# Performance work log

Hardware: AMD Instinct MI355X
Metric: run time of the kernel (lower is better)

Reference implementation:

```python
import jax, jax.numpy as jnp
import numpy as np

N = 8192
D_IN = 128
D_HID = 256  # hard-coded nn.Linear(input_dim, 256) in the module
D_OUT = 64
BN_EPS = 1e-5
LEAKY_SLOPE = 0.01


def setup_inputs() -> dict:
    key = jax.random.key(0)
    k_h, k_a, k_wt, k_wo = jax.random.split(key, 4)
    H = jax.random.normal(k_h, (N, D_IN), dtype=jnp.float32)
    # Fixed adjacency passed to __init__; values in [0,1) so mask=ceil(A*1e-5) is {0,1}
    A = jax.random.uniform(k_a, (N, N), dtype=jnp.float32)
    bn_weight = jnp.ones((D_IN,), jnp.float32)
    bn_bias = jnp.zeros((D_IN,), jnp.float32)
    W_theta = jax.random.normal(k_wt, (D_IN, D_HID), jnp.float32) * np.float32(1.0 / np.sqrt(D_IN))
    b_theta = jnp.zeros((D_HID,), jnp.float32)
    W_out = jax.random.normal(k_wo, (D_IN, D_OUT), jnp.float32) * np.float32(1.0 / np.sqrt(D_IN))
    b_out = jnp.zeros((D_OUT,), jnp.float32)
    return {"H": H, "A": A, "bn_weight": bn_weight, "bn_bias": bn_bias,
            "W_theta": W_theta, "b_theta": b_theta, "W_out": W_out, "b_out": b_out}


def reference(H, A, bn_weight, bn_bias, W_theta, b_theta, W_out, b_out):
    # BatchNorm1d in training mode: biased batch statistics over the node dim
    mean = jnp.mean(H, axis=0)
    var = jnp.mean(jnp.square(H - mean), axis=0)
    Hn = (H - mean) * jax.lax.rsqrt(var + BN_EPS) * bn_weight + bn_bias  # [N, D_IN]

    Hx = Hn @ W_theta + b_theta  # [N, 256]
    mask = jnp.ceil(A * 1e-5)    # constant {0,1} mask from fixed adjacency

    # Dynamic adjacency: clamp(sigmoid(Hx Hx^T), min=0.1) * mask + I
    S = jnp.clip(jax.nn.sigmoid(Hx @ Hx.T), 0.1, None)  # [N, N]
    Ad = S * mask + jnp.eye(N, dtype=H.dtype)

    # D^{-1/2} A D^{-1/2} via broadcast scaling (same math as diag matmuls)
    d = jax.lax.rsqrt(jnp.sum(Ad, axis=1))  # D^{-0.5}, [N]
    A_hat = Ad * d[:, None] * d[None, :]

    out = A_hat @ (Hn @ W_out + b_out)       # [N, D_OUT]
    out = jnp.where(out >= 0, out, LEAKY_SLOPE * out)  # LeakyReLU(0.01)
    return out, A_hat
```

## Files before the change

kernel.cpp:

```cpp
#include <hip/hip_runtime.h>
#include <hip/hip_bf16.h>

#define N 8192
#define DIN 128
#define DHID 256
#define DOUT 64
#define VP 136

typedef __attribute__((ext_vector_type(8))) short short8;
typedef __attribute__((ext_vector_type(8))) unsigned short u16x8;
typedef __attribute__((ext_vector_type(4))) float f32x4;
typedef __attribute__((ext_vector_type(2))) unsigned long long u64x2;

typedef __attribute__((address_space(1))) const unsigned int GlbU32;
typedef __attribute__((address_space(3))) unsigned int LdsU32;

__device__ inline void gload16(const void* g, void* l) {
  __builtin_amdgcn_global_load_lds((GlbU32*)g, (LdsU32*)l, 16, 0, 0);
}

#define LGKM_BAR()                                            \
  do {                                                        \
    asm volatile("s_waitcnt lgkmcnt(0)" ::: "memory");        \
    __builtin_amdgcn_sched_barrier(0);                        \
    __builtin_amdgcn_s_barrier();                             \
    __builtin_amdgcn_sched_barrier(0);                        \
  } while (0)

__device__ inline unsigned short f2bf(float x) {
  unsigned u = __float_as_uint(x);
  u += 0x7FFF + ((u >> 16) & 1);
  return (unsigned short)(u >> 16);
}
__device__ inline float bf2f(unsigned short u) {
  return __uint_as_float(((unsigned)u) << 16);
}
__device__ inline float sig_clip(float x) {
  float s = 1.0f / (1.0f + __expf(-x));
  return fmaxf(s, 0.1f);
}

__global__ __launch_bounds__(256) void maskpack(const float* __restrict__ A,
                                                unsigned long long* __restrict__ Mb) {
  size_t i = (size_t)blockIdx.x * 256 + threadIdx.x;
  size_t step = (size_t)gridDim.x * 256;
  int l = threadIdx.x & 63;
  for (; i < (size_t)N * N / 4; i += step) {
    f32x4 a = *(const f32x4*)&A[i * 4];
    unsigned long long b0 = __ballot(a[0] > 0.f);
    unsigned long long b1 = __ballot(a[1] > 0.f);
    unsigned long long b2 = __ballot(a[2] > 0.f);
    unsigned long long b3 = __ballot(a[3] > 0.f);
    size_t g = (i - l) >> 6;
    if (l < 4) {
      unsigned long long bb = (l == 0) ? b0 : (l == 1) ? b1 : (l == 2) ? b2 : b3;
      Mb[g * 4 + l] = bb;
    }
  }
}

__global__ void bn_stats(const float* __restrict__ H, const float* __restrict__ bnw,
                         const float* __restrict__ bnb, float* __restrict__ scale,
                         float* __restrict__ shift) {
  int f = blockIdx.x;
  int t = threadIdx.x;
  float s = 0.f, sq = 0.f;
  for (int r = t; r < N; r += 256) {
    float v = H[(size_t)r * DIN + f];
    s += v; sq += v * v;
  }
  __shared__ float ss[256], s2[256];
  ss[t] = s; s2[t] = sq;
  __syncthreads();
  for (int o = 128; o > 0; o >>= 1) {
    if (t < o) { ss[t] += ss[t + o]; s2[t] += s2[t + o]; }
    __syncthreads();
  }
  if (t == 0) {
    float mean = ss[0] * (1.0f / N);
    float var = s2[0] * (1.0f / N) - mean * mean;
    float sc = rsqrtf(var + 1e-5f) * bnw[f];
    scale[f] = sc;
    shift[f] = bnb[f] - mean * sc;
  }
}

__global__ __launch_bounds__(256) void proj(const float* __restrict__ H,
                     const float* __restrict__ scale, const float* __restrict__ shift,
                     const float* __restrict__ Wt, const float* __restrict__ bt,
                     const float* __restrict__ Wo, const float* __restrict__ bo,
                     unsigned short* __restrict__ Hx, unsigned short* __restrict__ M2T) {
  __shared__ float hn[8][DIN];
  int i0 = blockIdx.x * 8;
  int t = threadIdx.x;
  #pragma unroll
  for (int rep = 0; rep < 4; ++rep) {
    int idx = rep * 256 + t;
    int r = idx >> 7, c = idx & 127;
    float h = H[(size_t)(i0 + r) * DIN + c];
    hn[r][c] = fmaf(h, scale[c], shift[c]);
  }
  __syncthreads();
  {
    int c = t;
    float acc[8];
    float b = bt[c];
    #pragma unroll
    for (int r = 0; r < 8; ++r) acc[r] = b;
    for (int k = 0; k < DIN; ++k) {
      float w = Wt[k * DHID + c];
      #pragma unroll
      for (int r = 0; r < 8; ++r) acc[r] = fmaf(hn[r][k], w, acc[r]);
    }
    #pragma unroll
    for (int r = 0; r < 8; ++r) Hx[(size_t)(i0 + r) * DHID + c] = f2bf(acc[r]);
  }
  if (t < DOUT) {
    int c = t;
    float acc[8];
    float b = bo[c];
    #pragma unroll
    for (int r = 0; r < 8; ++r) acc[r] = b;
    for (int k = 0; k < DIN; ++k) {
      float w = Wo[k * DOUT + c];
      #pragma unroll
      for (int r = 0; r < 8; ++r) acc[r] = fmaf(hn[r][k], w, acc[r]);
    }
    u16x8 v;
    #pragma unroll
    for (int r = 0; r < 8; ++r) v[r] = f2bf(acc[r]);
    *(u16x8*)&M2T[(size_t)c * N + i0] = v;
  }
}

__global__ __launch_bounds__(256, 3) void rsum(const unsigned short* __restrict__ Hx,
                     const unsigned long long* __restrict__ Mb,
                     float* __restrict__ rowsum) {
  __shared__ unsigned short lsh[24576];
  __shared__ unsigned mbt32[64][4];
  unsigned short* lA = lsh;
  unsigned short* lb = lsh + 16384;
  const int blk = blockIdx.x;
  const int jq = blk & 7;
  const int it = blk >> 3;
  const int i0 = it * 64;
  const int t = threadIdx.x;
  const int w = t >> 6, l = t & 63;
  const int lr = l & 15, lg = l >> 4;
  const int srow = l >> 3;
  const int scol = ((l & 7) ^ srow) * 8;
  const int fswz = (lr & 7) * 8;

  #pragma unroll
  for (int itr = 0; itr < 8; ++itr) {
    int idx = itr * 4 + w;
    int c4 = idx >> 3, rg = idx & 7;
    int row = rg * 8 + srow;
    gload16(&Hx[(size_t)(i0 + row) * DHID + c4 * 64 + scol], &lA[idx * 512]);
  }
  if (t < 128) {
    int j0 = jq * 1024;
    int mrow = t >> 1, ep = (t & 1) * 2;
    u64x2 mv = *(const u64x2*)&Mb[(size_t)(i0 + mrow) * (N / 64) + (j0 >> 8) * 4 + ep];
    int sh = (j0 & 128) ? 32 : 0;
    mbt32[mrow][ep] = (unsigned)(mv[0] >> sh);
    mbt32[mrow][ep + 1] = (unsigned)(mv[1] >> sh);
  }
  __syncthreads();

  float rs[4] = {0.f, 0.f, 0.f, 0.f};
  f32x4 zero = {0.f, 0.f, 0.f, 0.f};

  for (int jtl = 0; jtl < 8; ++jtl) {
    const int j0 = (jq * 8 + jtl) * 128;
    f32x4 acc[8];
    #pragma unroll
    for (int n = 0; n < 8; ++n) acc[n] = zero;

    #pragma unroll
    for (int c4 = 0; c4 < 4; ++c4) {
      __syncthreads();
      #pragma unroll
      for (int itr = 0; itr < 4; ++itr) {
        int rg = itr * 4 + w;
        int row = rg * 8 + srow;
        gload16(&Hx[(size_t)(j0 + row) * DHID + c4 * 64 + scol], &lb[rg * 512]);
      }
      __syncthreads();
      #pragma unroll
      for (int kk = 0; kk < 2; ++kk) {
        int c = (kk * 32 + lg * 8) ^ fswz;
        short8 a0 = *(const short8*)&lA[c4 * 4096 + (w * 16 + lr) * 64 + c];
        short8 bf[8];
        #pragma unroll
        for (int n = 0; n < 8; ++n)
          bf[n] = *(const short8*)&lb[(n * 16 + lr) * 64 + c];
        #pragma unroll
        for (int n = 0; n < 8; ++n)
          acc[n] = __builtin_amdgcn_mfma_f32_16x16x32_bf16(a0, bf[n], acc[n], 0, 0, 0);
      }
    }

    #pragma unroll
    for (int r = 0; r < 4; ++r) {
      int rl = w * 16 + lg * 4 + r;
      int gi = i0 + rl;
      unsigned mw = mbt32[rl][lr & 3];
      float part = 0.f;
      #pragma unroll
      for (int n = 0; n < 8; ++n) {
        int gj = j0 + n * 16 + lr;
        float ms = ((mw >> (n * 4 + (lr >> 2))) & 1u) ? 1.f : 0.f;
        part += sig_clip(acc[n][r]) * ms + (gi == gj ? 1.f : 0.f);
      }
      rs[r] += part;
    }
    __syncthreads();
    if (jtl < 7 && t < 128) {
      int nj0 = (jq * 8 + jtl + 1) * 128;
      int mrow = t >> 1, ep = (t & 1) * 2;
      u64x2 mv = *(const u64x2*)&Mb[(size_t)(i0 + mrow) * (N / 64) + (nj0 >> 8) * 4 + ep];
      int sh = (nj0 & 128) ? 32 : 0;
      mbt32[mrow][ep] = (unsigned)(mv[0] >> sh);
      mbt32[mrow][ep + 1] = (unsigned)(mv[1] >> sh);
    }
  }

  #pragma unroll
  for (int r = 0; r < 4; ++r) {
    float p = rs[r];
    p += __shfl_xor(p, 1);
    p += __shfl_xor(p, 2);
    p += __shfl_xor(p, 4);
    p += __shfl_xor(p, 8);
    if (lr == 0) atomicAdd(&rowsum[i0 + w * 16 + lg * 4 + r], p);
  }
}

__global__ void dfin(float* rs) {
  int i = blockIdx.x * 256 + threadIdx.x;
  if (i < N) rs[i] = rsqrtf(rs[i]);
}

__global__ __launch_bounds__(256, 2) void finmm(const unsigned short* __restrict__ Hx,
                     const unsigned long long* __restrict__ Mb,
                     const float* __restrict__ dd,
                     const unsigned short* __restrict__ M2T,
                     float* __restrict__ Ahat, float* __restrict__ out) {
  __shared__ unsigned short lsh[33280];
  __shared__ unsigned mbt32[64][4];
  unsigned short* lA = lsh;
  unsigned short* lb = lsh + 16384;
  unsigned short* lVb = lsh + 24576;
  const int blk = blockIdx.x;
  const int jq = blk & 15;
  const int it = blk >> 4;
  const int i0 = it * 64;
  const int t = threadIdx.x;
  const int w = t >> 6, l = t & 63;
  const int lr = l & 15, lg = l >> 4;
  const int srow = l >> 3;
  const int scol = ((l & 7) ^ srow) * 8;
  const int fswz = (lr & 7) * 8;

  #pragma unroll
  for (int itr = 0; itr < 8; ++itr) {
    int idx = itr * 4 + w;
    int c4 = idx >> 3, rg = idx & 7;
    int row = rg * 8 + srow;
    gload16(&Hx[(size_t)(i0 + row) * DHID + c4 * 64 + scol], &lA[idx * 512]);
  }
  if (t < 128) {
    int j0 = jq * 512;
    int mrow = t >> 1, ep = (t & 1) * 2;
    u64x2 mv = *(const u64x2*)&Mb[(size_t)(i0 + mrow) * (N / 64) + (j0 >> 8) * 4 + ep];
    int sh = (j0 & 128) ? 32 : 0;
    mbt32[mrow][ep] = (unsigned)(mv[0] >> sh);
    mbt32[mrow][ep + 1] = (unsigned)(mv[1] >> sh);
  }
  __syncthreads();

  float di[4];
  #pragma unroll
  for (int r = 0; r < 4; ++r) di[r] = dd[i0 + w * 16 + lg * 4 + r];

  f32x4 acc2[4];
  f32x4 zero = {0.f, 0.f, 0.f, 0.f};
  #pragma unroll
  for (int n = 0; n < 4; ++n) acc2[n] = zero;

  for (int jtl = 0; jtl < 4; ++jtl) {
    const int j0 = (jq * 4 + jtl) * 128;
    f32x4 acc[8];
    #pragma unroll
    for (int n = 0; n < 8; ++n) acc[n] = zero;

    #pragma unroll
    for (int c4 = 0; c4 < 4; ++c4) {
      __syncthreads();
      #pragma unroll
      for (int itr = 0; itr < 4; ++itr) {
        int rg = itr * 4 + w;
        int row = rg * 8 + srow;
        gload16(&Hx[(size_t)(j0 + row) * DHID + c4 * 64 + scol], &lb[rg * 512]);
      }
      __syncthreads();
      #pragma unroll
      for (int kk = 0; kk < 2; ++kk) {
        int c = (kk * 32 + lg * 8) ^ fswz;
        short8 a0 = *(const short8*)&lA[c4 * 4096 + (w * 16 + lr) * 64 + c];
        short8 bf[8];
        #pragma unroll
        for (int n = 0; n < 8; ++n)
          bf[n] = *(const short8*)&lb[(n * 16 + lr) * 64 + c];
        #pragma unroll
        for (int n = 0; n < 8; ++n)
          acc[n] = __builtin_amdgcn_mfma_f32_16x16x32_bf16(a0, bf[n], acc[n], 0, 0, 0);
      }
    }

    float dj[8];
    #pragma unroll
    for (int n = 0; n < 8; ++n) dj[n] = dd[j0 + n * 16 + lr];
    #pragma unroll
    for (int r = 0; r < 4; ++r) {
      int rl = w * 16 + lg * 4 + r;
      int gi = i0 + rl;
      unsigned mw = mbt32[rl][lr & 3];
      #pragma unroll
      for (int n = 0; n < 8; ++n) {
        int gj = j0 + n * 16 + lr;
        float ms = ((mw >> (n * 4 + (lr >> 2))) & 1u) ? 1.f : 0.f;
        float v = sig_clip(acc[n][r]) * ms + (gi == gj ? 1.f : 0.f);
        float a = v * di[r] * dj[n];
        lVb[rl * VP + n * 16 + lr] = f2bf(a);
      }
    }
    LGKM_BAR();

    #pragma unroll
    for (int pass = 0; pass < 4; ++pass) {
      int row = pass * 16 + (t >> 4);
      int cc = (t & 15) * 8;
      u16x8 vv = *(const u16x8*)&lVb[row * VP + cc];
      f32x4 o0, o1;
      o0[0] = bf2f(vv[0]); o0[1] = bf2f(vv[1]); o0[2] = bf2f(vv[2]); o0[3] = bf2f(vv[3]);
      o1[0] = bf2f(vv[4]); o1[1] = bf2f(vv[5]); o1[2] = bf2f(vv[6]); o1[3] = bf2f(vv[7]);
      size_t idx = (size_t)(i0 + row) * N + j0 + cc;
      *(f32x4*)&Ahat[idx] = o0;
      *(f32x4*)&Ahat[idx + 4] = o1;
    }

    #pragma unroll
    for (int kk2 = 0; kk2 < 4; ++kk2) {
      short8 af2 = *(const short8*)&lVb[(w * 16 + lr) * VP + kk2 * 32 + lg * 8];
      short8 bfr[4];
      #pragma unroll
      for (int n = 0; n < 4; ++n)
        bfr[n] = *(const short8*)&M2T[(size_t)(n * 16 + lr) * N + j0 + kk2 * 32 + lg * 8];
      #pragma unroll
      for (int n = 0; n < 4; ++n)
        acc2[n] = __builtin_amdgcn_mfma_f32_16x16x32_bf16(af2, bfr[n], acc2[n], 0, 0, 0);
    }

    if (jtl < 3 && t < 128) {
      int nj0 = (jq * 4 + jtl + 1) * 128;
      int mrow = t >> 1, ep = (t & 1) * 2;
      u64x2 mv = *(const u64x2*)&Mb[(size_t)(i0 + mrow) * (N / 64) + (nj0 >> 8) * 4 + ep];
      int sh = (nj0 & 128) ? 32 : 0;
      mbt32[mrow][ep] = (unsigned)(mv[0] >> sh);
      mbt32[mrow][ep + 1] = (unsigned)(mv[1] >> sh);
    }
  }

  #pragma unroll
  for (int n = 0; n < 4; ++n)
    #pragma unroll
    for (int r = 0; r < 4; ++r) {
      int gi = i0 + w * 16 + lg * 4 + r;
      int gc = n * 16 + lr;
      atomicAdd(&out[(size_t)gi * DOUT + gc], acc2[n][r]);
    }
}

__global__ void leaky(float* out) {
  int i = blockIdx.x * 256 + threadIdx.x;
  if (i < N * DOUT) {
    float x = out[i];
    out[i] = x >= 0.f ? x : 0.01f * x;
  }
}

extern "C" void kernel_launch(void* const* d_in, const int* in_sizes, int n_in,
                              void* d_out, int out_size, void* d_ws, size_t ws_size,
                              hipStream_t stream) {
  const float* H   = (const float*)d_in[0];
  const float* A   = (const float*)d_in[1];
  const float* bnw = (const float*)d_in[2];
  const float* bnb = (const float*)d_in[3];
  const float* Wt  = (const float*)d_in[4];
  const float* bt  = (const float*)d_in[5];
  const float* Wo  = (const float*)d_in[6];
  const float* bo  = (const float*)d_in[7];
  float* out = (float*)d_out;
  float* Ahat = out + (size_t)N * DOUT;

  char* ws = (char*)d_ws;
  float* scale  = (float*)(ws + 0);
  float* shift  = (float*)(ws + 512);
  float* rowsum = (float*)(ws + 4096);
  unsigned short* M2T = (unsigned short*)(ws + 65536);
  unsigned short* Hx  = (unsigned short*)(ws + 2097152);
  unsigned long long* Mb = (unsigned long long*)(ws + (size_t)(6u << 20));

  hipMemsetAsync(rowsum, 0, N * sizeof(float), stream);
  hipMemsetAsync(out, 0, (size_t)N * DOUT * sizeof(float), stream);

  maskpack<<<4096, 256, 0, stream>>>(A, Mb);
  bn_stats<<<DIN, 256, 0, stream>>>(H, bnw, bnb, scale, shift);
  proj<<<N / 8, 256, 0, stream>>>(H, scale, shift, Wt, bt, Wo, bo, Hx, M2T);
  rsum<<<1024, 256, 0, stream>>>(Hx, Mb, rowsum);
  dfin<<<N / 256, 256, 0, stream>>>(rowsum);
  finmm<<<2048, 256, 0, stream>>>(Hx, Mb, rowsum, M2T, Ahat, out);
  leaky<<<(N * DOUT + 255) / 256, 256, 0, stream>>>(out);
}
```

Baseline: 369.9 us.

## Merge rowsum and final matmul into templated double-buffered band kernel

Replaces the separate rsum and finmm kernels with one templated kernel that processes 64-wide column tiles instead of 128. The Hx B-tile is double-buffered in LDS and the next chunk is prefetched with async global-to-LDS loads, synchronised by vmcnt-counted barriers instead of full __syncthreads pairs. The mask words are also fetched asynchronously into LDS. This aims to hide global load latency and improve occupancy through a smaller register and LDS footprint. The cost is more barriers per tile and fragile hand-tuned vmcnt counts.

```diff
diff --git a/kernel.cpp b/kernel.cpp
--- a/kernel.cpp
+++ b/kernel.cpp
@@ -5,12 +5,10 @@
 #define DIN 128
 #define DHID 256
 #define DOUT 64
-#define VP 136
 
 typedef __attribute__((ext_vector_type(8))) short short8;
 typedef __attribute__((ext_vector_type(8))) unsigned short u16x8;
 typedef __attribute__((ext_vector_type(4))) float f32x4;
-typedef __attribute__((ext_vector_type(2))) unsigned long long u64x2;
 
 typedef __attribute__((address_space(1))) const unsigned int GlbU32;
 typedef __attribute__((address_space(3))) unsigned int LdsU32;
@@ -22,6 +20,14 @@
 #define LGKM_BAR()                                            \
   do {                                                        \
     asm volatile("s_waitcnt lgkmcnt(0)" ::: "memory");        \
+    __builtin_amdgcn_sched_barrier(0);                        \
+    __builtin_amdgcn_s_barrier();                             \
+    __builtin_amdgcn_sched_barrier(0);                        \
+  } while (0)
+
+#define VM_BAR(nstr)                                          \
+  do {                                                        \
+    asm volatile("s_waitcnt vmcnt(" nstr ")" ::: "memory");   \
     __builtin_amdgcn_sched_barrier(0);                        \
     __builtin_amdgcn_s_barrier();                             \
     __builtin_amdgcn_sched_barrier(0);                        \
@@ -133,16 +139,22 @@
   }
 }
 
-__global__ __launch_bounds__(256, 3) void rsum(const unsigned short* __restrict__ Hx,
+template <int DOPV, int LT>
+__global__ __launch_bounds__(256, 2) void sband(const unsigned short* __restrict__ Hx,
                      const unsigned long long* __restrict__ Mb,
+                     const float* __restrict__ dd,
+                     const unsigned short* __restrict__ M2T,
+                     float* __restrict__ Ahat, float* __restrict__ out,
                      float* __restrict__ rowsum) {
-  __shared__ unsigned short lsh[24576];
+  __shared__ unsigned short lsh[DOPV ? 30208 : 25600];
   __shared__ unsigned mbt32[64][4];
-  unsigned short* lA = lsh;
-  unsigned short* lb = lsh + 16384;
+  const int LB0 = 16384, LB1 = 20480;
+  const int LVB = 24576;
+  const int MST = DOPV ? 29184 : 24576;
   const int blk = blockIdx.x;
-  const int jq = blk & 7;
-  const int it = blk >> 3;
+  const int NB = DOPV ? 16 : 8;
+  const int jq = blk & (NB - 1);
+  const int it = blk >> (DOPV ? 4 : 3);
   const int i0 = it * 64;
   const int t = threadIdx.x;
   const int w = t >> 6, l = t & 63;
@@ -150,237 +162,166 @@
   const int srow = l >> 3;
   const int scol = ((l & 7) ^ srow) * 8;
   const int fswz = (lr & 7) * 8;
+  const int th = t & 127;
 
   #pragma unroll
   for (int itr = 0; itr < 8; ++itr) {
     int idx = itr * 4 + w;
-    int c4 = idx >> 3, rg = idx & 7;
+    int c4i = idx >> 3, rg = idx & 7;
     int row = rg * 8 + srow;
-    gload16(&Hx[(size_t)(i0 + row) * DHID + c4 * 64 + scol], &lA[idx * 512]);
-  }
-  if (t < 128) {
-    int j0 = jq * 1024;
-    int mrow = t >> 1, ep = (t & 1) * 2;
-    u64x2 mv = *(const u64x2*)&Mb[(size_t)(i0 + mrow) * (N / 64) + (j0 >> 8) * 4 + ep];
-    int sh = (j0 & 128) ? 32 : 0;
-    mbt32[mrow][ep] = (unsigned)(mv[0] >> sh);
-    mbt32[mrow][ep + 1] = (unsigned)(mv[1] >> sh);
-  }
-  __syncthreads();
+    gload16(&Hx[(size_t)(i0 + row) * DHID + c4i * 64 + scol], &lsh[idx * 512]);
+  }
+  {
+    int j00 = jq * LT * 64;
+    gload16(&Mb[(size_t)(i0 + (th >> 1)) * 128 + (size_t)(j00 >> 8) * 4 + (th & 1) * 2],
+            &lsh[MST + (w & 1) * 512]);
+    #pragma unroll
+    for (int itr = 0; itr < 2; ++itr) {
+      int rg = itr * 4 + w;
+      int row = rg * 8 + srow;
+      gload16(&Hx[(size_t)(j00 + row) * DHID + scol], &lsh[LB0 + rg * 512]);
+    }
+  }
+  float di[4];
+  if (DOPV) {
+    #pragma unroll
+    for (int r = 0; r < 4; ++r) di[r] = dd[i0 + w * 16 + lg * 4 + r];
+  }
+  VM_BAR("0");
 
   float rs[4] = {0.f, 0.f, 0.f, 0.f};
+  f32x4 acc2[4];
   f32x4 zero = {0.f, 0.f, 0.f, 0.f};
-
-  for (int jtl = 0; jtl < 8; ++jtl) {
-    const int j0 = (jq * 8 + jtl) * 128;
-    f32x4 acc[8];
-    #pragma unroll
-    for (int n = 0; n < 8; ++n) acc[n] = zero;
+  #pragma unroll
+  for (int n = 0; n < 4; ++n) acc2[n] = zero;
+
+  for (int tt = 0; tt < LT; ++tt) {
+    const int j0 = (jq * LT + tt) * 64;
+    f32x4 acc[4];
+    #pragma unroll
+    for (int n = 0; n < 4; ++n) acc[n] = zero;
 
     #pragma unroll
     for (int c4 = 0; c4 < 4; ++c4) {
-      __syncthreads();
-      #pragma unroll
-      for (int itr = 0; itr < 4; ++itr) {
-        int rg = itr * 4 + w;
-        int row = rg * 8 + srow;
-        gload16(&Hx[(size_t)(j0 + row) * DHID + c4 * 64 + scol], &lb[rg * 512]);
-      }
-      __syncthreads();
+      bool isLast = (tt == LT - 1) && (c4 == 3);
+      if (!isLast) {
+        int njt = (c4 == 3) ? tt + 1 : tt;
+        int nc4 = (c4 + 1) & 3;
+        int nj0 = (jq * LT + njt) * 64;
+        int dstoff = (c4 & 1) ? LB0 : LB1;
+        #pragma unroll
+        for (int itr = 0; itr < 2; ++itr) {
+          int rg = itr * 4 + w;
+          int row = rg * 8 + srow;
+          gload16(&Hx[(size_t)(nj0 + row) * DHID + nc4 * 64 + scol], &lsh[dstoff + rg * 512]);
+        }
+      }
+      if (c4 == 0)      { if (DOPV) VM_BAR("17"); else VM_BAR("3"); }
+      else if (c4 == 3) { if (tt < LT - 1) VM_BAR("2"); else VM_BAR("0"); }
+      else              VM_BAR("2");
+      const int curoff = (c4 & 1) ? LB1 : LB0;
       #pragma unroll
       for (int kk = 0; kk < 2; ++kk) {
         int c = (kk * 32 + lg * 8) ^ fswz;
-        short8 a0 = *(const short8*)&lA[c4 * 4096 + (w * 16 + lr) * 64 + c];
-        short8 bf[8];
-        #pragma unroll
-        for (int n = 0; n < 8; ++n)
-          bf[n] = *(const short8*)&lb[(n * 16 + lr) * 64 + c];
-        #pragma unroll
-        for (int n = 0; n < 8; ++n)
+        short8 a0 = *(const short8*)&lsh[c4 * 4096 + (w * 16 + lr) * 64 + c];
+        short8 bf[4];
+        #pragma unroll
+        for (int n = 0; n < 4; ++n)
+          bf[n] = *(const short8*)&lsh[curoff + (n * 16 + lr) * 64 + c];
+        #pragma unroll
+        for (int n = 0; n < 4; ++n)
           acc[n] = __builtin_amdgcn_mfma_f32_16x16x32_bf16(a0, bf[n], acc[n], 0, 0, 0);
       }
-    }
-
+      LGKM_BAR();
+    }
+
+    {
+      int crow = t >> 2, ce = t & 3;
+      unsigned long long cv = *(const unsigned long long*)&lsh[MST + crow * 16 + ce * 4];
+      int sh = (j0 & 192) >> 2;
+      mbt32[crow][ce] = (unsigned)((cv >> sh) & 0xFFFFull);
+    }
+    LGKM_BAR();
+
+    float dj[4];
+    if (DOPV) {
+      #pragma unroll
+      for (int n = 0; n < 4; ++n) dj[n] = dd[j0 + n * 16 + lr];
+    }
     #pragma unroll
     for (int r = 0; r < 4; ++r) {
       int rl = w * 16 + lg * 4 + r;
       int gi = i0 + rl;
       unsigned mw = mbt32[rl][lr & 3];
-      float part = 0.f;
-      #pragma unroll
-      for (int n = 0; n < 8; ++n) {
+      #pragma unroll
+      for (int n = 0; n < 4; ++n) {
         int gj = j0 + n * 16 + lr;
         float ms = ((mw >> (n * 4 + (lr >> 2))) & 1u) ? 1.f : 0.f;
-        part += sig_clip(acc[n][r]) * ms + (gi == gj ? 1.f : 0.f);
-      }
-      rs[r] += part;
-    }
-    __syncthreads();
-    if (jtl < 7 && t < 128) {
-      int nj0 = (jq * 8 + jtl + 1) * 128;
-      int mrow = t >> 1, ep = (t & 1) * 2;
-      u64x2 mv = *(const u64x2*)&Mb[(size_t)(i0 + mrow) * (N / 64) + (nj0 >> 8) * 4 + ep];
-      int sh = (nj0 & 128) ? 32 : 0;
-      mbt32[mrow][ep] = (unsigned)(mv[0] >> sh);
-      mbt32[mrow][ep + 1] = (unsigned)(mv[1] >> sh);
-    }
-  }
-
-  #pragma unroll
-  for (int r = 0; r < 4; ++r) {
-    float p = rs[r];
-    p += __shfl_xor(p, 1);
-    p += __shfl_xor(p, 2);
-    p += __shfl_xor(p, 4);
-    p += __shfl_xor(p, 8);
-    if (lr == 0) atomicAdd(&rowsum[i0 + w * 16 + lg * 4 + r], p);
+        float v = sig_clip(acc[n][r]) * ms + (gi == gj ? 1.f : 0.f);
+        if (DOPV)
+          lsh[LVB + rl * 72 + n * 16 + lr] = f2bf(v * di[r] * dj[n]);
+        else
+          rs[r] += v;
+      }
+    }
+    if (tt < LT - 1) {
+      int nj0 = (jq * LT + tt + 1) * 64;
+      gload16(&Mb[(size_t)(i0 + (th >> 1)) * 128 + (size_t)(nj0 >> 8) * 4 + (th & 1) * 2],
+              &lsh[MST + (w & 1) * 512]);
+    }
+
+    if (DOPV) {
+      LGKM_BAR();
+      #pragma unroll
+      for (int kk2 = 0; kk2 < 2; ++kk2) {
+        short8 a2 = *(const short8*)&lsh[LVB + (w * 16 + lr) * 72 + kk2 * 32 + lg * 8];
+        short8 br[4];
+        #pragma unroll
+        for (int n = 0; n < 4; ++n)
+          br[n] = *(const short8*)&M2T[(size_t)(n * 16 + lr) * N + j0 + kk2 * 32 + lg * 8];
+        #pragma unroll
+        for (int n = 0; n < 4; ++n)
+          acc2[n] = __builtin_amdgcn_mfma_f32_16x16x32_bf16(a2, br[n], acc2[n], 0, 0, 0);
+      }
+      #pragma unroll
+      for (int p = 0; p < 2; ++p) {
+        int row = p * 32 + (t >> 3);
+        int cc = (t & 7) * 8;
+        u16x8 vv = *(const u16x8*)&lsh[LVB + row * 72 + cc];
+        f32x4 o0, o1;
+        o0[0] = bf2f(vv[0]); o0[1] = bf2f(vv[1]); o0[2] = bf2f(vv[2]); o0[3] = bf2f(vv[3]);
+        o1[0] = bf2f(vv[4]); o1[1] = bf2f(vv[5]); o1[2] = bf2f(vv[6]); o1[3] = bf2f(vv[7]);
+        size_t idx = (size_t)(i0 + row) * N + j0 + cc;
+        *(f32x4*)&Ahat[idx] = o0;
+        *(f32x4*)&Ahat[idx + 4] = o1;
+      }
+    }
+  }
+
+  if (DOPV) {
+    #pragma unroll
+    for (int n = 0; n < 4; ++n)
+      #pragma unroll
+      for (int r = 0; r < 4; ++r) {
+        int gi = i0 + w * 16 + lg * 4 + r;
+        atomicAdd(&out[(size_t)gi * DOUT + n * 16 + lr], acc2[n][r]);
+      }
+  } else {
+    #pragma unroll
+    for (int r = 0; r < 4; ++r) {
+      float p = rs[r];
+      p += __shfl_xor(p, 1);
+      p += __shfl_xor(p, 2);
+      p += __shfl_xor(p, 4);
+      p += __shfl_xor(p, 8);
+      if (lr == 0) atomicAdd(&rowsum[i0 + w * 16 + lg * 4 + r], p);
+    }
   }
 }
 
 __global__ void dfin(float* rs) {
   int i = blockIdx.x * 256 + threadIdx.x;
   if (i < N) rs[i] = rsqrtf(rs[i]);
-}
-
-__global__ __launch_bounds__(256, 2) void finmm(const unsigned short* __restrict__ Hx,
-                     const unsigned long long* __restrict__ Mb,
-                     const float* __restrict__ dd,
-                     const unsigned short* __restrict__ M2T,
-                     float* __restrict__ Ahat, float* __restrict__ out) {
-  __shared__ unsigned short lsh[33280];
-  __shared__ unsigned mbt32[64][4];
-  unsigned short* lA = lsh;
-  unsigned short* lb = lsh + 16384;
-  unsigned short* lVb = lsh + 24576;
-  const int blk = blockIdx.x;
-  const int jq = blk & 15;
-  const int it = blk >> 4;
-  const int i0 = it * 64;
-  const int t = threadIdx.x;
-  const int w = t >> 6, l = t & 63;
-  const int lr = l & 15, lg = l >> 4;
-  const int srow = l >> 3;
-  const int scol = ((l & 7) ^ srow) * 8;
-  const int fswz = (lr & 7) * 8;
-
-  #pragma unroll
-  for (int itr = 0; itr < 8; ++itr) {
-    int idx = itr * 4 + w;
-    int c4 = idx >> 3, rg = idx & 7;
-    int row = rg * 8 + srow;
-    gload16(&Hx[(size_t)(i0 + row) * DHID + c4 * 64 + scol], &lA[idx * 512]);
-  }
-  if (t < 128) {
-    int j0 = jq * 512;
-    int mrow = t >> 1, ep = (t & 1) * 2;
-    u64x2 mv = *(const u64x2*)&Mb[(size_t)(i0 + mrow) * (N / 64) + (j0 >> 8) * 4 + ep];
-    int sh = (j0 & 128) ? 32 : 0;
-    mbt32[mrow][ep] = (unsigned)(mv[0] >> sh);
-    mbt32[mrow][ep + 1] = (unsigned)(mv[1] >> sh);
-  }
-  __syncthreads();
-
-  float di[4];
-  #pragma unroll
-  for (int r = 0; r < 4; ++r) di[r] = dd[i0 + w * 16 + lg * 4 + r];
-
-  f32x4 acc2[4];
-  f32x4 zero = {0.f, 0.f, 0.f, 0.f};
-  #pragma unroll
-  for (int n = 0; n < 4; ++n) acc2[n] = zero;
-
-  for (int jtl = 0; jtl < 4; ++jtl) {
-    const int j0 = (jq * 4 + jtl) * 128;
-    f32x4 acc[8];
-    #pragma unroll
-    for (int n = 0; n < 8; ++n) acc[n] = zero;
-
-    #pragma unroll
-    for (int c4 = 0; c4 < 4; ++c4) {
-      __syncthreads();
-      #pragma unroll
-      for (int itr = 0; itr < 4; ++itr) {
-        int rg = itr * 4 + w;
-        int row = rg * 8 + srow;
-        gload16(&Hx[(size_t)(j0 + row) * DHID + c4 * 64 + scol], &lb[rg * 512]);
-      }
-      __syncthreads();
-      #pragma unroll
-      for (int kk = 0; kk < 2; ++kk) {
-        int c = (kk * 32 + lg * 8) ^ fswz;
-        short8 a0 = *(const short8*)&lA[c4 * 4096 + (w * 16 + lr) * 64 + c];
-        short8 bf[8];
-        #pragma unroll
-        for (int n = 0; n < 8; ++n)
-          bf[n] = *(const short8*)&lb[(n * 16 + lr) * 64 + c];
-        #pragma unroll
-        for (int n = 0; n < 8; ++n)
-          acc[n] = __builtin_amdgcn_mfma_f32_16x16x32_bf16(a0, bf[n], acc[n], 0, 0, 0);
-      }
-    }
-
-    float dj[8];
-    #pragma unroll
-    for (int n = 0; n < 8; ++n) dj[n] = dd[j0 + n * 16 + lr];
-    #pragma unroll
-    for (int r = 0; r < 4; ++r) {
-      int rl = w * 16 + lg * 4 + r;
-      int gi = i0 + rl;
-      unsigned mw = mbt32[rl][lr & 3];
-      #pragma unroll
-      for (int n = 0; n < 8; ++n) {
-        int gj = j0 + n * 16 + lr;
-        float ms = ((mw >> (n * 4 + (lr >> 2))) & 1u) ? 1.f : 0.f;
-        float v = sig_clip(acc[n][r]) * ms + (gi == gj ? 1.f : 0.f);
-        float a = v * di[r] * dj[n];
-        lVb[rl * VP + n * 16 + lr] = f2bf(a);
-      }
-    }
-    LGKM_BAR();
-
-    #pragma unroll
-    for (int pass = 0; pass < 4; ++pass) {
-      int row = pass * 16 + (t >> 4);
-      int cc = (t & 15) * 8;
-      u16x8 vv = *(const u16x8*)&lVb[row * VP + cc];
-      f32x4 o0, o1;
-      o0[0] = bf2f(vv[0]); o0[1] = bf2f(vv[1]); o0[2] = bf2f(vv[2]); o0[3] = bf2f(vv[3]);
-      o1[0] = bf2f(vv[4]); o1[1] = bf2f(vv[5]); o1[2] = bf2f(vv[6]); o1[3] = bf2f(vv[7]);
-      size_t idx = (size_t)(i0 + row) * N + j0 + cc;
-      *(f32x4*)&Ahat[idx] = o0;
-      *(f32x4*)&Ahat[idx + 4] = o1;
-    }
-
-    #pragma unroll
-    for (int kk2 = 0; kk2 < 4; ++kk2) {
-      short8 af2 = *(const short8*)&lVb[(w * 16 + lr) * VP + kk2 * 32 + lg * 8];
-      short8 bfr[4];
-      #pragma unroll
-      for (int n = 0; n < 4; ++n)
-        bfr[n] = *(const short8*)&M2T[(size_t)(n * 16 + lr) * N + j0 + kk2 * 32 + lg * 8];
-      #pragma unroll
-      for (int n = 0; n < 4; ++n)
-        acc2[n] = __builtin_amdgcn_mfma_f32_16x16x32_bf16(af2, bfr[n], acc2[n], 0, 0, 0);
-    }
-
-    if (jtl < 3 && t < 128) {
-      int nj0 = (jq * 4 + jtl + 1) * 128;
-      int mrow = t >> 1, ep = (t & 1) * 2;
-      u64x2 mv = *(const u64x2*)&Mb[(size_t)(i0 + mrow) * (N / 64) + (nj0 >> 8) * 4 + ep];
-      int sh = (nj0 & 128) ? 32 : 0;
-      mbt32[mrow][ep] = (unsigned)(mv[0] >> sh);
-      mbt32[mrow][ep + 1] = (unsigned)(mv[1] >> sh);
-    }
-  }
-
-  #pragma unroll
-  for (int n = 0; n < 4; ++n)
-    #pragma unroll
-    for (int r = 0; r < 4; ++r) {
-      int gi = i0 + w * 16 + lg * 4 + r;
-      int gc = n * 16 + lr;
-      atomicAdd(&out[(size_t)gi * DOUT + gc], acc2[n][r]);
-    }
 }
 
 __global__ void leaky(float* out) {
@@ -419,8 +360,8 @@
   maskpack<<<4096, 256, 0, stream>>>(A, Mb);
   bn_stats<<<DIN, 256, 0, stream>>>(H, bnw, bnb, scale, shift);
   proj<<<N / 8, 256, 0, stream>>>(H, scale, shift, Wt, bt, Wo, bo, Hx, M2T);
-  rsum<<<1024, 256, 0, stream>>>(Hx, Mb, rowsum);
+  sband<0, 16><<<1024, 256, 0, stream>>>(Hx, Mb, nullptr, nullptr, nullptr, nullptr, rowsum);
   dfin<<<N / 256, 256, 0, stream>>>(rowsum);
-  finmm<<<2048, 256, 0, stream>>>(Hx, Mb, rowsum, M2T, Ahat, out);
+  sband<1, 8><<<2048, 256, 0, stream>>>(Hx, Mb, rowsum, M2T, Ahat, out, nullptr);
   leaky<<<(N * DOUT + 255) / 256, 256, 0, stream>>>(out);
 }
```

After: 381.8 us. +3.2%, slower.
